# Kernel optimization log

Measured on AMD Instinct MI355X. Metric: run time of the kernel, lower is better.

The kernel has to match this reference:

```python
import jax, jax.numpy as jnp
import numpy as np

TOPK = 16          # static stand-in for dense_to_sparse(A_virtual): top-k neighbors per master node
LAMBDA_ATTN = 1.0  # VirtualGeneration temperature
GAMMA = 4.0        # gaussian radial basis width
R_CENTERS = 8      # radial_embedding.out_dim
NEG = -1e9


def _sh(v):
    # stand-in spherical harmonics: 16 monomials (lmax=3-ish) of the unit direction
    n = jnp.linalg.norm(v, axis=-1, keepdims=True)
    u = v / (n + 1e-9)
    x, y, z = u[:, 0], u[:, 1], u[:, 2]
    o = jnp.ones_like(x)
    return jnp.stack([o, x, y, z, x * x, y * y, z * z, x * y, x * z, y * z,
                      x * x * x, y * y * y, z * z * z, x * x * y, y * y * z, z * z * x], axis=-1)


def _radial(r):
    # gaussian radial basis, r: [E,1] -> [E,R]
    centers = jnp.linspace(0.0, 5.0, R_CENTERS, dtype=r.dtype)
    return jnp.exp(-GAMMA * (r - centers[None, :]) ** 2)


def _msgs(x, src, dst, sh, feats, Wr, wsh, n):
    # MACE-style conv message aggregation: radial-gated, SH-modulated gather/scatter
    gate = feats @ Wr                               # [E, Cin]
    msg = x[src] * gate * (sh @ wsh)[:, None]       # [E, Cin]
    return jax.ops.segment_sum(msg, dst, num_segments=n)


def _forward(h, pos, edge_index, edge_sh, edge_feats,
             W_loc_r, w_loc_sh, W_loc_out, W_prod_loc,
             W_ms1, b_ms1, W_ms2, b_ms2, Wq, Wk,
             W_a1, b_a1, W_a2, b_a2,
             W_h_r, w_h_sh, W_h_out, W_prod_h):
    N, D = h.shape
    D2 = W_loc_out.shape[1]
    S = W_ms1.shape[0]
    src, dst = edge_index[0], edge_index[1]

    # --- local conv + prod skip (h_local) ---
    h_up = _msgs(h, src, dst, edge_sh, edge_feats, W_loc_r, w_loc_sh, N) @ W_loc_out  # [N, D2]
    h_local = h_up @ W_prod_loc + jnp.pad(h, ((0, 0), (0, D2 - D)))
    h_scalar = h_local[:, :S]

    # --- master selection (MLP -> sigmoid -> hard threshold) ---
    m = jax.nn.sigmoid(jax.nn.relu(h_scalar @ W_ms1 + b_ms1) @ W_ms2 + b_ms2)[:, 0]
    mf = (m > 0.5).astype(h.dtype)

    # --- induced master-master edges: mask instead of dynamic subgraph extraction ---
    pair = mf[src] * mf[dst]
    vec_i = pos[src] - pos[dst]
    len_i = jnp.linalg.norm(vec_i, axis=-1, keepdims=True)
    sh_i = _sh(vec_i)
    rf_i = _radial(len_i) * pair[:, None]  # induced full_weights == 1, masked to master pairs

    # --- virtual edge generation: dense attention scores among masters, static top-k ---
    q = h_scalar @ Wq
    kk = h_scalar @ Wk
    scores_nn = (q @ kk.T) / (np.sqrt(S).astype(np.float32) * LAMBDA_ATTN)  # [N, N]
    pair_ok = (mf[:, None] * mf[None, :]) * (1.0 - jnp.eye(N, dtype=h.dtype))  # no self loops
    scores_nn = jnp.where(pair_ok > 0, scores_nn, NEG)
    topv, topi = jax.lax.top_k(scores_nn, TOPK)        # [N, K]
    vsrc = jnp.repeat(jnp.arange(N), TOPK)             # [N*K]
    vdst = topi.reshape(-1)
    vvalid = (topv.reshape(-1) > NEG / 2).astype(h.dtype)

    vec_v = pos[vsrc] - pos[vdst]
    len_v = jnp.linalg.norm(vec_v, axis=-1, keepdims=True)
    sh_v = _sh(vec_v)
    rf_v = _radial(len_v)

    # --- scatter-softmax attention over virtual edges (per destination) ---
    attn_in = jnp.concatenate([h_scalar[vsrc], h_scalar[vdst], rf_v], axis=-1)
    sc = (jax.nn.relu(attn_in @ W_a1 + b_a1) @ W_a2 + b_a2)[:, 0]
    sc = jnp.where(vvalid > 0, sc, NEG)
    mx = jax.ops.segment_max(sc, vdst, num_segments=N)
    ex = jnp.where(vvalid > 0, jnp.exp(sc - mx[vdst]), 0.0)
    den = jax.ops.segment_sum(ex, vdst, num_segments=N)
    wv = ex / (den[vdst] + 1e-12)
    rf_v = rf_v * wv[:, None]

    # --- hierarchical conv over induced + virtual master edges ---
    agg = (_msgs(h_local, src, dst, sh_i, rf_i, W_h_r, w_h_sh, N)
           + _msgs(h_local, vsrc, vdst, sh_v, rf_v, W_h_r, w_h_sh, N))
    h_m_up = agg @ W_h_out
    h_hier = (h_m_up @ W_prod_h + h_local) * mf[:, None]  # zero at non-master slots

    # --- gated combine ---
    return (1.0 - m)[:, None] * h_local + m[:, None] * h_hier


def setup_inputs():
    key = jax.random.key(0)
    ks = jax.random.split(key, 24)
    N, E, D, D2, S, R, L, HID = 4096, 131072, 128, 256, 128, 8, 16, 64

    def w(k, shape):
        return (jax.random.normal(k, shape, jnp.float32) / np.sqrt(shape[0]).astype(np.float32))

    return dict(
        h=jax.random.normal(ks[0], (N, D), jnp.float32),
        pos=jax.random.normal(ks[1], (N, 3), jnp.float32),
        edge_index=jax.random.randint(ks[2], (2, E), 0, N),
        edge_sh=jax.random.normal(ks[3], (E, L), jnp.float32),
        edge_feats=jax.random.normal(ks[4], (E, R), jnp.float32),
        batch=jnp.zeros((N,), jnp.int32),
        W_loc_r=w(ks[5], (R, D)),
        w_loc_sh=jax.random.normal(ks[6], (L,), jnp.float32) / 4.0,
        W_loc_out=w(ks[7], (D, D2)),
        W_prod_loc=w(ks[8], (D2, D2)),
        W_ms1=w(ks[9], (S, HID)), b_ms1=jnp.zeros((HID,), jnp.float32),
        W_ms2=w(ks[10], (HID, 1)), b_ms2=jnp.zeros((1,), jnp.float32),
        Wq=w(ks[11], (S, S)), Wk=w(ks[12], (S, S)),
        W_a1=w(ks[13], (2 * S + R, S)), b_a1=jnp.zeros((S,), jnp.float32),
        W_a2=w(ks[14], (S, 1)), b_a2=jnp.zeros((1,), jnp.float32),
        W_h_r=w(ks[15], (R, D2)),
        w_h_sh=jax.random.normal(ks[16], (L,), jnp.float32) / 4.0,
        W_h_out=w(ks[17], (D2, D2)),
        W_prod_h=w(ks[18], (D2, D2)),
    )


def reference(h, pos, edge_index, edge_sh, edge_feats, batch,
              W_loc_r, w_loc_sh, W_loc_out, W_prod_loc,
              W_ms1, b_ms1, W_ms2, b_ms2, Wq, Wk,
              W_a1, b_a1, W_a2, b_a2,
              W_h_r, w_h_sh, W_h_out, W_prod_h):
    # batch is unused by the original forward as well
    return _forward(h, pos, edge_index, edge_sh, edge_feats,
                    W_loc_r, w_loc_sh, W_loc_out, W_prod_loc,
                    W_ms1, b_ms1, W_ms2, b_ms2, Wq, Wk,
                    W_a1, b_a1, W_a2, b_a2,
                    W_h_r, w_h_sh, W_h_out, W_prod_h)
```

## Files before the change

### kernel.cpp

```cpp
#include <hip/hip_runtime.h>

typedef unsigned int u32;
typedef unsigned long long u64;

#define NN 4096
#define EE 131072
#define DD 128
#define D2 256
#define SS 128
#define RR 8
#define LL 16
#define HH 64
#define TK 16
#define VSTRIDE 32
#define VV2 (NN*VSTRIDE)
#define NEGF -1000000000.0f
#define MNEGF -3.0e38f
#define SCLF 11.313708305358886719f
#define DELTA 1.0e-3f
#define CHUNK 1024
#define RCH 32
#define VCH 64
#define MAXCH_R 8192
#define MAXCH_V 5184

__device__ __forceinline__ float fadd(float a, float b) { return __fadd_rn(a, b); }
__device__ __forceinline__ float fsub(float a, float b) { return __fsub_rn(a, b); }
__device__ __forceinline__ float fmul(float a, float b) { return __fmul_rn(a, b); }
__device__ __forceinline__ float ffma(float a, float b, float c) { return __fmaf_rn(a, b, c); }

enum : size_t {
  B_CNTR   = 0,
  B_CNTV   = 16384,
  B_MXE    = 32768,
  ZERO_END = 49152,
  B_STARTR = 49152,
  B_STARTV = 69632,
  B_LISTR  = 90112,
  B_LISTV  = 614400,
  B_TOPI   = 1138688,
  B_WFAC   = 1662976,
  B_AMSG   = 2187264,
  B_HUP    = 4284416,
  B_HLOC   = 8478720,
  B_T1     = 12673024,
  B_MARR   = 13721600,
  B_MF     = 13737984,
  B_Q      = 13754368,
  B_KT     = 15851520,
  B_SC     = 17948672,
  B_WV     = 18472960,
  B_SUMR   = 18997248,
  B_SUMV   = 23191552,
  B_AGG    = 27385856,
  B_HMUP   = 31580160,
  B_CURR   = 35774464,
  B_CURV   = 35790848,
  B_P1     = 35807232,
  B_P2     = 37904384,
  B_TOTAL  = 40001536,
  B_ERP    = B_Q,
  B_EVP    = B_HUP,
  B_SHV1   = B_SUMR,
  B_SCHUNK = B_SUMR,
  B_CHT    = B_HUP + 3145728,
  O_CHJV   = 64,
  O_CHPV   = 64 + 4*MAXCH_V,
  O_CHJR   = 64 + 8*MAXCH_V,
  O_CHPR   = 64 + 8*MAXCH_V + 4*MAXCH_R,
  B_CHT2   = 40001536,
  B_SBIG   = 41943040,
  WS_BIG   = 109051904
};

__global__ void count_keys(const int* __restrict__ keys, int n, u32* __restrict__ cnt) {
  int e = blockIdx.x * 256 + threadIdx.x;
  if (e >= n) return;
  int d = keys[e];
  if (d >= 0) atomicAdd(&cnt[d], 1u);
}

__global__ __launch_bounds__(256) void scan_ex_par(const u32* __restrict__ cnt,
                                                   u32* __restrict__ start,
                                                   u32* __restrict__ cursor, int n,
                                                   int csz, u32* __restrict__ chCnt,
                                                   int* __restrict__ chJ,
                                                   int* __restrict__ chP) {
  __shared__ u32 part[256];
  __shared__ u32 cpart[256];
  int t = threadIdx.x;
  int per = n / 256;
  u32 s = 0;
  for (int i = 0; i < per; ++i) s += cnt[t*per + i];
  part[t] = s;
  __syncthreads();
  if (t == 0) {
    u32 run = 0;
    for (int i = 0; i < 256; ++i) { u32 v = part[i]; part[i] = run; run += v; }
    start[n] = run;
  }
  __syncthreads();
  u32 run = part[t];
  for (int i = 0; i < per; ++i) {
    int k = t*per + i;
    start[k] = run;
    cursor[k] = run;
    run += cnt[k];
  }
  if (csz > 0) {
    u32 cc = 0;
    for (int i = 0; i < per; ++i) {
      u32 len = cnt[t*per + i];
      cc += (len + (u32)csz - 1u) / (u32)csz;
    }
    cpart[t] = cc;
    __syncthreads();
    if (t == 0) {
      u32 r2 = 0;
      for (int i = 0; i < 256; ++i) { u32 v = cpart[i]; cpart[i] = r2; r2 += v; }
      *chCnt = r2;
    }
    __syncthreads();
    u32 b = cpart[t];
    u32 sb = part[t];
    for (int i = 0; i < per; ++i) {
      int k = t*per + i;
      u32 len = cnt[k];
      u32 nch = (len + (u32)csz - 1u) / (u32)csz;
      for (u32 kk = 0; kk < nch; ++kk) { chJ[b] = k; chP[b] = (int)(sb + kk*(u32)csz); ++b; }
      sb += len;
    }
  }
}

__global__ void fill_atomic(const int* __restrict__ keys, int n,
                            u32* __restrict__ cursor, int* __restrict__ list) {
  int e = blockIdx.x * 256 + threadIdx.x;
  if (e >= n) return;
  int d = keys[e];
  if (d < 0) return;
  u32 p = atomicAdd(&cursor[d], 1u);
  list[p] = e;
}

__global__ void build_chunks(const u32* __restrict__ start, int nseg, int csz,
                             u32* __restrict__ cnt, int* __restrict__ chJ,
                             int* __restrict__ chP) {
  int j = blockIdx.x * 256 + threadIdx.x;
  if (j >= nseg) return;
  u32 s0 = start[j], s1 = start[j + 1];
  if (s0 >= s1) return;
  int nch = (int)((s1 - s0) + (u32)csz - 1) / csz;
  u32 b = atomicAdd(cnt, (u32)nch);
  for (int k = 0; k < nch; ++k) {
    chJ[b + k] = j;
    chP[b + k] = (int)(s0 + (u32)k * (u32)csz);
  }
}

__global__ void edge_pre1(const float* __restrict__ esh, const float* __restrict__ wsh,
                          float* __restrict__ shv1) {
  int e = blockIdx.x * 256 + threadIdx.x;
  if (e >= EE) return;
  float s = 0.f;
  #pragma unroll
  for (int l = 0; l < LL; ++l) s = ffma(esh[e*LL + l], wsh[l], s);
  shv1[e] = s;
}

__global__ __launch_bounds__(128) void rep_msgs1(
    const float* __restrict__ h, const int* __restrict__ ei,
    const float* __restrict__ efeat,
    const float* __restrict__ Wr, const float* __restrict__ shv1,
    const u32* __restrict__ startR, const int* __restrict__ listR,
    float* __restrict__ amsg)
{
  __shared__ int   ssrc[64];
  __shared__ float sshv[64];
  __shared__ float sef[64][8];
  int d = blockIdx.x, c = threadIdx.x;
  float wr[RR];
  #pragma unroll
  for (int r = 0; r < RR; ++r) wr[r] = Wr[r*DD + c];
  float acc = 0.f;
  u32 s0 = startR[d], s1 = startR[d + 1];
  for (u32 t0 = s0; t0 < s1; t0 += 64) {
    int tl = (int)(s1 - t0 < 64u ? s1 - t0 : 64u);
    if (c < tl) {
      int e = listR[t0 + c];
      ssrc[c] = ei[e];
      sshv[c] = shv1[e];
      const float4* fe = reinterpret_cast<const float4*>(&efeat[(size_t)e*RR]);
      float4 f0 = fe[0], f1 = fe[1];
      sef[c][0]=f0.x; sef[c][1]=f0.y; sef[c][2]=f0.z; sef[c][3]=f0.w;
      sef[c][4]=f1.x; sef[c][5]=f1.y; sef[c][6]=f1.z; sef[c][7]=f1.w;
    }
    __syncthreads();
    int k = 0;
    for (; k + 4 <= tl; k += 4) {
      float h0 = h[(size_t)ssrc[k  ]*DD + c];
      float h1 = h[(size_t)ssrc[k+1]*DD + c];
      float h2 = h[(size_t)ssrc[k+2]*DD + c];
      float h3 = h[(size_t)ssrc[k+3]*DD + c];
      float g0 = 0.f, g1 = 0.f, g2 = 0.f, g3 = 0.f;
      #pragma unroll
      for (int r = 0; r < RR; ++r) {
        g0 = ffma(sef[k  ][r], wr[r], g0);
        g1 = ffma(sef[k+1][r], wr[r], g1);
        g2 = ffma(sef[k+2][r], wr[r], g2);
        g3 = ffma(sef[k+3][r], wr[r], g3);
      }
      acc = fadd(acc, fmul(fmul(h0, g0), sshv[k  ]));
      acc = fadd(acc, fmul(fmul(h1, g1), sshv[k+1]));
      acc = fadd(acc, fmul(fmul(h2, g2), sshv[k+2]));
      acc = fadd(acc, fmul(fmul(h3, g3), sshv[k+3]));
    }
    for (; k < tl; ++k) {
      float hv = h[(size_t)ssrc[k]*DD + c];
      float g = 0.f;
      #pragma unroll
      for (int r = 0; r < RR; ++r) g = ffma(sef[k][r], wr[r], g);
      acc = fadd(acc, fmul(fmul(hv, g), sshv[k]));
    }
    __syncthreads();
  }
  amsg[d*DD + c] = acc;
}

__global__ __launch_bounds__(256) void gemm64(
    const float* __restrict__ A, int lda,
    const float* __restrict__ B, int ldb,
    float* __restrict__ C, int ldc,
    int K, int mode,
    const float* __restrict__ x1,
    const float* __restrict__ marr, const float* __restrict__ mfarr,
    float* __restrict__ outp)
{
  __shared__ float As[16][68];
  __shared__ float Bs[16][68];
  int tid = threadIdx.x;
  int bm = blockIdx.x << 6, bn = blockIdx.y << 6;
  int tm = ((tid >> 4) << 2), tn = ((tid & 15) << 2);
  float acc[4][4] = {};
  for (int k0 = 0; k0 < K; k0 += 16) {
    #pragma unroll
    for (int t = 0; t < 4; ++t) {
      int idx = tid + (t << 8);
      int r = idx >> 4, c = idx & 15;
      As[c][r] = A[(size_t)(bm + r)*lda + k0 + c];
      int rb = idx >> 6, cb = idx & 63;
      Bs[rb][cb] = B[(size_t)(k0 + rb)*ldb + bn + cb];
    }
    __syncthreads();
    #pragma unroll
    for (int kk = 0; kk < 16; ++kk) {
      float4 av = *reinterpret_cast<const float4*>(&As[kk][tm]);
      float4 bv = *reinterpret_cast<const float4*>(&Bs[kk][tn]);
      float a0 = av.x, a1 = av.y, a2 = av.z, a3 = av.w;
      float b0 = bv.x, b1 = bv.y, b2 = bv.z, b3 = bv.w;
      acc[0][0]=ffma(a0,b0,acc[0][0]); acc[0][1]=ffma(a0,b1,acc[0][1]);
      acc[0][2]=ffma(a0,b2,acc[0][2]); acc[0][3]=ffma(a0,b3,acc[0][3]);
      acc[1][0]=ffma(a1,b0,acc[1][0]); acc[1][1]=ffma(a1,b1,acc[1][1]);
      acc[1][2]=ffma(a1,b2,acc[1][2]); acc[1][3]=ffma(a1,b3,acc[1][3]);
      acc[2][0]=ffma(a2,b0,acc[2][0]); acc[2][1]=ffma(a2,b1,acc[2][1]);
      acc[2][2]=ffma(a2,b2,acc[2][2]); acc[2][3]=ffma(a2,b3,acc[2][3]);
      acc[3][0]=ffma(a3,b0,acc[3][0]); acc[3][1]=ffma(a3,b1,acc[3][1]);
      acc[3][2]=ffma(a3,b2,acc[3][2]); acc[3][3]=ffma(a3,b3,acc[3][3]);
    }
    __syncthreads();
  }
  #pragma unroll
  for (int ii = 0; ii < 4; ++ii) {
    int r = bm + tm + ii;
    #pragma unroll
    for (int jj = 0; jj < 4; ++jj) {
      int c = bn + tn + jj;
      float v = acc[ii][jj];
      if (mode == 0) {
        C[(size_t)r*ldc + c] = v;
      } else if (mode == 1) {
        if (c < DD) v = fadd(v, x1[(size_t)r*DD + c]);
        C[(size_t)r*ldc + c] = v;
      } else if (mode == 2) {
        float hl = x1[(size_t)r*D2 + c];
        float hh = fmul(fadd(v, hl), mfarr[r]);
        float m = marr[r];
        outp[(size_t)r*D2 + c] = fadd(fmul(fsub(1.f, m), hl), fmul(m, hh));
      } else {
        C[(size_t)c*ldc + r] = v;
      }
    }
  }
}

__global__ __launch_bounds__(256, 2) void gemm_score2(
    const float* __restrict__ A, const float* __restrict__ B,
    const float* __restrict__ mf, int rowoff,
    float* __restrict__ S)
{
  __shared__ float As[16][136];
  __shared__ float Bs[16][136];
  int tid = threadIdx.x;
  int bm = blockIdx.x << 7;
  int bn = blockIdx.y << 7;
  int tm = ((tid >> 4) << 2);
  int tn = ((tid & 15) << 2);
  float acc[8][8] = {};
  for (int k0 = 0; k0 < SS; k0 += 16) {
    {
      int row = tid >> 1, seg = (tid & 1) << 3;
      const float4 a0 = *reinterpret_cast<const float4*>(
          &A[(size_t)(bm + row)*SS + k0 + seg]);
      const float4 a1 = *reinterpret_cast<const float4*>(
          &A[(size_t)(bm + row)*SS + k0 + seg + 4]);
      As[seg+0][row] = a0.x; As[seg+1][row] = a0.y;
      As[seg+2][row] = a0.z; As[seg+3][row] = a0.w;
      As[seg+4][row] = a1.x; As[seg+5][row] = a1.y;
      As[seg+6][row] = a1.z; As[seg+7][row] = a1.w;
    }
    #pragma unroll
    for (int t = 0; t < 2; ++t) {
      int f = tid + (t << 8);
      int rb = f >> 5, cb = (f & 31) << 2;
      const float4 bv = *reinterpret_cast<const float4*>(
          &B[(size_t)(k0 + rb)*NN + bn + cb]);
      *reinterpret_cast<float4*>(&Bs[rb][cb]) = bv;
    }
    __syncthreads();
    #pragma unroll
    for (int kk = 0; kk < 16; ++kk) {
      float4 al = *reinterpret_cast<const float4*>(&As[kk][tm]);
      float4 ah = *reinterpret_cast<const float4*>(&As[kk][tm + 64]);
      float4 bl = *reinterpret_cast<const float4*>(&Bs[kk][tn]);
      float4 bh = *reinterpret_cast<const float4*>(&Bs[kk][tn + 64]);
      float a[8] = {al.x, al.y, al.z, al.w, ah.x, ah.y, ah.z, ah.w};
      float b[8] = {bl.x, bl.y, bl.z, bl.w, bh.x, bh.y, bh.z, bh.w};
      #pragma unroll
      for (int i = 0; i < 8; ++i)
        #pragma unroll
        for (int j = 0; j < 8; ++j)
          acc[i][j] = ffma(a[i], b[j], acc[i][j]);
    }
    __syncthreads();
  }
  #pragma unroll
  for (int ii = 0; ii < 8; ++ii) {
    int r = bm + ((ii < 4) ? (tm + ii) : (tm + 64 + (ii - 4)));
    int rg = rowoff + r;
    #pragma unroll
    for (int jg = 0; jg < 2; ++jg) {
      int cb = bn + tn + (jg << 6);
      float4 ov;
      {
        float s0 = __fdiv_rn(acc[ii][4*jg+0], SCLF);
        float s1 = __fdiv_rn(acc[ii][4*jg+1], SCLF);
        float s2 = __fdiv_rn(acc[ii][4*jg+2], SCLF);
        float s3 = __fdiv_rn(acc[ii][4*jg+3], SCLF);
        ov.x = ((mf[cb+0] > 0.5f) && (cb+0 != rg)) ? s0 : NEGF;
        ov.y = ((mf[cb+1] > 0.5f) && (cb+1 != rg)) ? s1 : NEGF;
        ov.z = ((mf[cb+2] > 0.5f) && (cb+2 != rg)) ? s2 : NEGF;
        ov.w = ((mf[cb+3] > 0.5f) && (cb+3 != rg)) ? s3 : NEGF;
      }
      *reinterpret_cast<float4*>(&S[(size_t)r*NN + cb]) = ov;
    }
  }
}

__device__ __forceinline__ u64 enc_key(float v, int j) {
  u32 u = __float_as_uint(v);
  u = (u & 0x80000000u) ? ~u : (u | 0x80000000u);
  return ((u64)u << 32) | (u32)(0xFFFFFFFFu - (u32)j);
}
__device__ __forceinline__ float dec_val(u64 k) {
  u32 e = (u32)(k >> 32);
  u32 u = (e & 0x80000000u) ? (e ^ 0x80000000u) : ~e;
  return __uint_as_float(u);
}
__device__ __forceinline__ int dec_idx(u64 k) {
  return (int)(0xFFFFFFFFu - (u32)k);
}

__global__ __launch_bounds__(256) void rep_sel(
    const float* __restrict__ S, int rowoff, const float* __restrict__ mf,
    int* __restrict__ topi, float* __restrict__ wfac)
{
  __shared__ u64 wm[2][4];
  int tid = threadIdx.x;
  int row = rowoff + blockIdx.x;
  int base = row * VSTRIDE;
  if (mf[row] <= 0.5f) {
    if (tid < VSTRIDE) { topi[base + tid] = -1; wfac[base + tid] = 0.f; }
    return;
  }
  u64 kk[16];
  const float4* rp = reinterpret_cast<const float4*>(S + (size_t)blockIdx.x * NN);
  #pragma unroll
  for (int g = 0; g < 4; ++g) {
    float4 v = rp[tid + (g << 8)];
    int j0 = (tid << 2) + (g << 10);
    kk[4*g+0] = enc_key(v.x, j0);
    kk[4*g+1] = enc_key(v.y, j0 + 1);
    kk[4*g+2] = enc_key(v.z, j0 + 2);
    kk[4*g+3] = enc_key(v.w, j0 + 3);
  }
  u64 cmx = 0;
  #pragma unroll
  for (int i = 0; i < 16; ++i) cmx = (kk[i] > cmx) ? kk[i] : cmx;
  int w = tid >> 6;
  u64 rv = cmx;
  #pragma unroll
  for (int off = 32; off > 0; off >>= 1) {
    u64 o = __shfl_down(rv, off);
    if (o > rv) rv = o;
  }
  rv = __shfl(rv, 0);

  float v15 = 0.f, v16 = 0.f; int i15 = -1, i16 = -1;
  for (int it = 0; it < 17; ++it) {
    int p = it & 1;
    if ((tid & 63) == 0) wm[p][w] = rv;
    __syncthreads();
    u64 m0 = wm[p][0], m1 = wm[p][1], m2 = wm[p][2], m3 = wm[p][3];
    u64 g01 = (m0 > m1) ? m0 : m1;
    u64 g23 = (m2 > m3) ? m2 : m3;
    u64 gmax = (g01 > g23) ? g01 : g23;
    if (tid == 0) {
      float fv = dec_val(gmax);
      int fi = dec_idx(gmax);
      if (it < 15) {
        bool ok = fv > 0.5f * NEGF;
        topi[base + it] = ok ? fi : -1;
        wfac[base + it] = ok ? 1.f : 0.f;
      } else if (it == 15) { v15 = fv; i15 = fi; }
      else                 { v16 = fv; i16 = fi; }
    }
    if (rv == gmax) {
      if (cmx == gmax) {
        u64 nm = 0;
        #pragma unroll
        for (int i = 0; i < 16; ++i) {
          kk[i] = (kk[i] == gmax) ? 0ull : kk[i];
          nm = (kk[i] > nm) ? kk[i] : nm;
        }
        cmx = nm;
      }
      u64 r2 = cmx;
      #pragma unroll
      for (int off = 32; off > 0; off >>= 1) {
        u64 o = __shfl_down(r2, off);
        if (o > r2) r2 = o;
      }
      rv = __shfl(r2, 0);
    }
  }
  if (tid == 0) {
    bool b16 = v15 > 0.5f * NEGF;
    bool b17 = v16 > 0.5f * NEGF;
    bool contested = b16 && b17 && (fsub(v15, v16) < DELTA);
    topi[base + 15] = b16 ? i15 : -1;
    wfac[base + 15] = b16 ? (contested ? 0.5f : 1.f) : 0.f;
    topi[base + 16] = contested ? i16 : -1;
    wfac[base + 16] = contested ? 0.5f : 0.f;
  }
  if (tid >= 17 && tid < VSTRIDE) { topi[base + tid] = -1; wfac[base + tid] = 0.f; }
}

__global__ __launch_bounds__(64) void rep_mask(const float* __restrict__ t1,
    const float* __restrict__ b1, const float* __restrict__ W2,
    const float* __restrict__ b2, float* __restrict__ marr, float* __restrict__ mf)
{
  __shared__ float t3[HH];
  int n = blockIdx.x, hh = threadIdx.x;
  t3[hh] = fmaxf(fadd(t1[n*HH + hh], b1[hh]), 0.f);
  __syncthreads();
  if (hh == 0) {
    float acc = 0.f;
    for (int k = 0; k < HH; ++k) acc = ffma(t3[k], W2[k], acc);
    float z = fadd(acc, b2[0]);
    float m = __fdiv_rn(1.f, fadd(1.f, expf(-z)));
    marr[n] = m;
    mf[n] = (m > 0.5f) ? 1.f : 0.f;
  }
}

__device__ __forceinline__ float centerf(int r) {
  return (float)(((double)r * 5.0) / 7.0);
}

__global__ __launch_bounds__(256) void attn_edge2(
    const float* __restrict__ P1, const float* __restrict__ P2,
    const float* __restrict__ pos, const int* __restrict__ topi,
    const float* __restrict__ Wa1, const float* __restrict__ ba1,
    const float* __restrict__ Wa2, const float* __restrict__ ba2,
    float* __restrict__ sc, u32* __restrict__ mxe)
{
  __shared__ float wsum[4];
  __shared__ float srf[2][8];
  int tid = threadIdx.x;
  int eh = tid >> 7;
  int c = tid & 127;
  int idx = blockIdx.x * 2 + eh;
  int i = idx / 17;
  int k = idx - i * 17;
  int v = (i << 5) + k;
  int j = topi[v];
  if (c < 8 && j >= 0) {
    float vx = fsub(pos[i*3+0], pos[j*3+0]);
    float vy = fsub(pos[i*3+1], pos[j*3+1]);
    float vz = fsub(pos[i*3+2], pos[j*3+2]);
    float n2 = fadd(fadd(fmul(vx,vx), fmul(vy,vy)), fmul(vz,vz));
    float len = __fsqrt_rn(n2);
    float dr = fsub(len, centerf(c));
    srf[eh][c] = expf(fmul(-4.f, fmul(dr, dr)));
  }
  __syncthreads();
  float p = 0.f;
  if (j >= 0) {
    float t = fadd(P1[(size_t)i*SS + c], P2[(size_t)j*SS + c]);
    #pragma unroll
    for (int r = 0; r < RR; ++r) {
      t = ffma(srf[eh][r], Wa1[(256 + r)*SS + c], t);
    }
    t = fmaxf(fadd(t, ba1[c]), 0.f);
    p = fmul(t, Wa2[c]);
  }
  #pragma unroll
  for (int off = 32; off > 0; off >>= 1) p += __shfl_down(p, off);
  int wid = tid >> 6;
  if ((tid & 63) == 0) wsum[wid] = p;
  __syncthreads();
  if ((tid & 127) == 0 && j >= 0) {
    float acc = wsum[eh*2] + wsum[eh*2 + 1];
    float s = fadd(acc, ba2[0]);
    sc[v] = s;
    u32 u = __float_as_uint(s);
    u = (u & 0x80000000u) ? ~u : (u | 0x80000000u);
    atomicMax(&mxe[j], u);
  }
}

__global__ __launch_bounds__(64) void rep_denwv2(
    const float* __restrict__ sc, const u32* __restrict__ mxe,
    const u32* __restrict__ startV, const int* __restrict__ listV,
    const float* __restrict__ wfac, float* __restrict__ wvv)
{
  int j = blockIdx.x;
  int lane = threadIdx.x;
  u32 s0 = startV[j], s1 = startV[j + 1];
  if (s0 == s1) return;
  u32 ue = mxe[j];
  u32 b = (ue & 0x80000000u) ? (ue ^ 0x80000000u) : ~ue;
  float mx = __uint_as_float(b);
  float psum = 0.f;
  for (u32 idx = s0 + lane; idx < s1; idx += 64) {
    int v = listV[idx];
    float ex = fmul(wfac[v], expf(fsub(sc[v], mx)));
    wvv[v] = ex;
    psum += ex;
  }
  #pragma unroll
  for (int off = 32; off > 0; off >>= 1) psum += __shfl_down(psum, off);
  float den = __shfl(psum, 0);
  float dd = fadd(den, 1e-12f);
  for (u32 idx = s0 + lane; idx < s1; idx += 64) {
    int v = listV[idx];
    wvv[v] = __fdiv_rn(wvv[v], dd);
  }
}

__device__ __forceinline__ float shrep(float vx, float vy, float vz,
                                       const float* __restrict__ w) {
  float n2 = fadd(fadd(fmul(vx,vx), fmul(vy,vy)), fmul(vz,vz));
  float n = __fsqrt_rn(n2);
  float dnm = fadd(n, 1e-9f);
  float x = __fdiv_rn(vx, dnm), y = __fdiv_rn(vy, dnm), z = __fdiv_rn(vz, dnm);
  float t[16];
  t[0]=1.f; t[1]=x; t[2]=y; t[3]=z;
  t[4]=fmul(x,x); t[5]=fmul(y,y); t[6]=fmul(z,z);
  t[7]=fmul(x,y); t[8]=fmul(x,z); t[9]=fmul(y,z);
  t[10]=fmul(fmul(x,x),x); t[11]=fmul(fmul(y,y),y); t[12]=fmul(fmul(z,z),z);
  t[13]=fmul(fmul(x,x),y); t[14]=fmul(fmul(y,y),z); t[15]=fmul(fmul(z,z),x);
  float s = 0.f;
  #pragma unroll
  for (int l = 0; l < 16; ++l) s = ffma(t[l], w[l], s);
  return s;
}

__global__ void edge_pre_rv(const float* __restrict__ pos, const int* __restrict__ ei,
                            const float* __restrict__ mf, const float* __restrict__ whsh,
                            const int* __restrict__ listR, float* __restrict__ erp,
                            const int* __restrict__ topi, const float* __restrict__ wvv,
                            const u32* __restrict__ startV, const int* __restrict__ listV,
                            float* __restrict__ evp) {
  int b = blockIdx.x;
  if (b < EE/256) {
    int p = b * 256 + threadIdx.x;
    int e = listR[p];
    int src = ei[e], dst = ei[EE + e];
    float* op = erp + (size_t)p * 9;
    if (mf[src] <= 0.5f || mf[dst] <= 0.5f) {
      #pragma unroll
      for (int r = 0; r < 9; ++r) op[r] = 0.f;
      return;
    }
    float vx = fsub(pos[src*3+0], pos[dst*3+0]);
    float vy = fsub(pos[src*3+1], pos[dst*3+1]);
    float vz = fsub(pos[src*3+2], pos[dst*3+2]);
    op[0] = shrep(vx, vy, vz, whsh);
    float len = __fsqrt_rn(fadd(fadd(fmul(vx,vx), fmul(vy,vy)), fmul(vz,vz)));
    #pragma unroll
    for (int r = 0; r < RR; ++r) {
      float dr = fsub(len, centerf(r));
      op[1 + r] = expf(fmul(-4.f, fmul(dr, dr)));
    }
  } else {
    int p = (b - EE/256) * 256 + threadIdx.x;
    if (p >= (int)startV[NN]) return;
    int v = listV[p];
    int i = v >> 5;
    int j = topi[v];
    float w = wvv[v];
    float* op = evp + (size_t)p * 9;
    float vx = fsub(pos[i*3+0], pos[j*3+0]);
    float vy = fsub(pos[i*3+1], pos[j*3+1]);
    float vz = fsub(pos[i*3+2], pos[j*3+2]);
    op[0] = shrep(vx, vy, vz, whsh);
    float len = __fsqrt_rn(fadd(fadd(fmul(vx,vx), fmul(vy,vy)), fmul(vz,vz)));
    #pragma unroll
    for (int r = 0; r < RR; ++r) {
      float dr = fsub(len, centerf(r));
      op[1 + r] = fmul(expf(fmul(-4.f, fmul(dr, dr))), w);
    }
  }
}

__global__ __launch_bounds__(256) void rep_msgs2r4(
    const float* __restrict__ hloc, const int* __restrict__ ei,
    const float* __restrict__ Whr, const float* __restrict__ erp,
    const u32* __restrict__ startR, const int* __restrict__ listR,
    const u32* __restrict__ cnt, const int* __restrict__ chJ,
    const int* __restrict__ chP, float* __restrict__ sumR)
{
  __shared__ int   ssrc[RCH];
  __shared__ float sep[RCH][9];
  int b = blockIdx.x;
  if (b >= (int)(*cnt)) return;
  int d = chJ[b], c = threadIdx.x;
  u32 p0 = (u32)chP[b];
  u32 p1 = startR[d + 1];
  u32 pe = p0 + RCH; if (pe < p1) p1 = pe;
  int len = (int)(p1 - p0);
  if (c < len) ssrc[c] = ei[listR[p0 + c]];
  for (int t = c; t < len*9; t += 256) (&sep[0][0])[t] = erp[(size_t)p0*9 + t];
  __syncthreads();
  float whr[RR];
  #pragma unroll
  for (int r = 0; r < RR; ++r) whr[r] = Whr[r*D2 + c];
  float acc = 0.f;
  int k = 0;
  for (; k + 4 <= len; k += 4) {
    float h0 = hloc[(size_t)ssrc[k  ]*D2 + c];
    float h1 = hloc[(size_t)ssrc[k+1]*D2 + c];
    float h2 = hloc[(size_t)ssrc[k+2]*D2 + c];
    float h3 = hloc[(size_t)ssrc[k+3]*D2 + c];
    float g0 = 0.f, g1 = 0.f, g2 = 0.f, g3 = 0.f;
    #pragma unroll
    for (int r = 0; r < RR; ++r) {
      g0 = ffma(sep[k  ][1 + r], whr[r], g0);
      g1 = ffma(sep[k+1][1 + r], whr[r], g1);
      g2 = ffma(sep[k+2][1 + r], whr[r], g2);
      g3 = ffma(sep[k+3][1 + r], whr[r], g3);
    }
    acc = fadd(acc, fmul(fmul(h0, g0), sep[k  ][0]));
    acc = fadd(acc, fmul(fmul(h1, g1), sep[k+1][0]));
    acc = fadd(acc, fmul(fmul(h2, g2), sep[k+2][0]));
    acc = fadd(acc, fmul(fmul(h3, g3), sep[k+3][0]));
  }
  for (; k < len; ++k) {
    float hv = hloc[(size_t)ssrc[k]*D2 + c];
    float g = 0.f;
    #pragma unroll
    for (int r = 0; r < RR; ++r) g = ffma(sep[k][1 + r], whr[r], g);
    acc = fadd(acc, fmul(fmul(hv, g), sep[k][0]));
  }
  atomicAdd(&sumR[(size_t)d*D2 + c], acc);
}

__global__ __launch_bounds__(256) void rep_msgs2v4(
    const float* __restrict__ hloc, const int* __restrict__ listV,
    const float* __restrict__ Whr, const float* __restrict__ evp,
    const u32* __restrict__ startV,
    const u32* __restrict__ cnt, const int* __restrict__ chJ,
    const int* __restrict__ chP, float* __restrict__ sumR)
{
  __shared__ int   si[VCH];
  __shared__ float sep[VCH][9];
  int b = blockIdx.x;
  if (b >= (int)(*cnt)) return;
  int j = chJ[b], c = threadIdx.x;
  u32 p0 = (u32)chP[b];
  u32 p1 = startV[j + 1];
  u32 pe = p0 + VCH; if (pe < p1) p1 = pe;
  int len = (int)(p1 - p0);
  if (c < len) si[c] = listV[p0 + c] >> 5;
  for (int t = c; t < len*9; t += 256) (&sep[0][0])[t] = evp[(size_t)p0*9 + t];
  __syncthreads();
  float whr[RR];
  #pragma unroll
  for (int r = 0; r < RR; ++r) whr[r] = Whr[r*D2 + c];
  float acc = 0.f;
  int k = 0;
  for (; k + 4 <= len; k += 4) {
    float h0 = hloc[(size_t)si[k  ]*D2 + c];
    float h1 = hloc[(size_t)si[k+1]*D2 + c];
    float h2 = hloc[(size_t)si[k+2]*D2 + c];
    float h3 = hloc[(size_t)si[k+3]*D2 + c];
    float g0 = 0.f, g1 = 0.f, g2 = 0.f, g3 = 0.f;
    #pragma unroll
    for (int r = 0; r < RR; ++r) {
      g0 = ffma(sep[k  ][1 + r], whr[r], g0);
      g1 = ffma(sep[k+1][1 + r], whr[r], g1);
      g2 = ffma(sep[k+2][1 + r], whr[r], g2);
      g3 = ffma(sep[k+3][1 + r], whr[r], g3);
    }
    acc = fadd(acc, fmul(fmul(h0, g0), sep[k  ][0]));
    acc = fadd(acc, fmul(fmul(h1, g1), sep[k+1][0]));
    acc = fadd(acc, fmul(fmul(h2, g2), sep[k+2][0]));
    acc = fadd(acc, fmul(fmul(h3, g3), sep[k+3][0]));
  }
  for (; k < len; ++k) {
    float hv = hloc[(size_t)si[k]*D2 + c];
    float g = 0.f;
    #pragma unroll
    for (int r = 0; r < RR; ++r) g = ffma(sep[k][1 + r], whr[r], g);
    acc = fadd(acc, fmul(fmul(hv, g), sep[k][0]));
  }
  atomicAdd(&sumR[(size_t)j*D2 + c], acc);
}

extern "C" void kernel_launch(void* const* d_in, const int* in_sizes, int n_in,
                              void* d_out, int out_size, void* d_ws, size_t ws_size,
                              hipStream_t stream)
{
  char* wsb = (char*)d_ws;
  const float* h     = (const float*)d_in[0];
  const float* pos   = (const float*)d_in[1];
  const int*   ei    = (const int*)d_in[2];
  const float* esh   = (const float*)d_in[3];
  const float* efeat = (const float*)d_in[4];
  const float* Wlr   = (const float*)d_in[6];
  const float* wlsh  = (const float*)d_in[7];
  const float* Wlo   = (const float*)d_in[8];
  const float* Wpl   = (const float*)d_in[9];
  const float* Wms1  = (const float*)d_in[10];
  const float* bms1  = (const float*)d_in[11];
  const float* Wms2  = (const float*)d_in[12];
  const float* bms2  = (const float*)d_in[13];
  const float* Wq    = (const float*)d_in[14];
  const float* Wk    = (const float*)d_in[15];
  const float* Wa1   = (const float*)d_in[16];
  const float* ba1   = (const float*)d_in[17];
  const float* Wa2   = (const float*)d_in[18];
  const float* ba2   = (const float*)d_in[19];
  const float* Whr   = (const float*)d_in[20];
  const float* whsh  = (const float*)d_in[21];
  const float* Who   = (const float*)d_in[22];
  const float* Wph   = (const float*)d_in[23];

  u32* cntR   = (u32*)(wsb + B_CNTR);
  u32* cntV   = (u32*)(wsb + B_CNTV);
  u32* mxe    = (u32*)(wsb + B_MXE);
  u32* startR = (u32*)(wsb + B_STARTR);
  u32* startV = (u32*)(wsb + B_STARTV);
  u32* curR   = (u32*)(wsb + B_CURR);
  u32* curV   = (u32*)(wsb + B_CURV);
  int* listR  = (int*)(wsb + B_LISTR);
  int* listV  = (int*)(wsb + B_LISTV);
  int* topi   = (int*)(wsb + B_TOPI);
  float* wfac = (float*)(wsb + B_WFAC);
  float* amsg = (float*)(wsb + B_AMSG);
  float* hup  = (float*)(wsb + B_HUP);
  float* hloc = (float*)(wsb + B_HLOC);
  float* t1   = (float*)(wsb + B_T1);
  float* marr = (float*)(wsb + B_MARR);
  float* mf   = (float*)(wsb + B_MF);
  float* q    = (float*)(wsb + B_Q);
  float* kT   = (float*)(wsb + B_KT);
  float* sc   = (float*)(wsb + B_SC);
  float* wvv  = (float*)(wsb + B_WV);
  float* sumR = (float*)(wsb + B_SUMR);
  float* hmup = (float*)(wsb + B_HMUP);
  float* P1   = (float*)(wsb + B_P1);
  float* P2   = (float*)(wsb + B_P2);
  float* erp  = (float*)(wsb + B_ERP);
  float* evp  = (float*)(wsb + B_EVP);
  float* shv1 = (float*)(wsb + B_SHV1);

  const bool big = ws_size >= (size_t)WS_BIG;
  char* cht = wsb + (big ? B_CHT2 : B_CHT);
  u32* chCntV = (u32*)(cht);
  u32* chCntR = (u32*)(cht + 4);
  int* chJv   = (int*)(cht + O_CHJV);
  int* chPv   = (int*)(cht + O_CHPV);
  int* chJr   = (int*)(cht + O_CHJR);
  int* chPr   = (int*)(cht + O_CHPR);
  float* Sbuf = (float*)(wsb + (big ? B_SBIG : B_SCHUNK));

  hipMemsetAsync(d_ws, 0, ZERO_END, stream);

  count_keys<<<EE/256, 256, 0, stream>>>(ei + EE, EE, cntR);
  if (big)
    scan_ex_par<<<1, 256, 0, stream>>>(cntR, startR, curR, NN, RCH, chCntR, chJr, chPr);
  else
    scan_ex_par<<<1, 256, 0, stream>>>(cntR, startR, curR, NN, 0, nullptr, nullptr, nullptr);
  fill_atomic<<<EE/256, 256, 0, stream>>>(ei + EE, EE, curR, listR);

  edge_pre1<<<EE/256, 256, 0, stream>>>(esh, wlsh, shv1);
  rep_msgs1<<<NN, 128, 0, stream>>>(h, ei, efeat, Wlr, shv1, startR, listR, amsg);
  gemm64<<<dim3(64,4), 256, 0, stream>>>(amsg, DD, Wlo, D2, hup, D2, DD, 0,
                                         nullptr, nullptr, nullptr, nullptr);
  gemm64<<<dim3(64,4), 256, 0, stream>>>(hup, D2, Wpl, D2, hloc, D2, D2, 1,
                                         h, nullptr, nullptr, nullptr);
  gemm64<<<dim3(64,1), 256, 0, stream>>>(hloc, D2, Wms1, HH, t1, HH, SS, 0,
                                         nullptr, nullptr, nullptr, nullptr);
  rep_mask<<<NN, 64, 0, stream>>>(t1, bms1, Wms2, bms2, marr, mf);
  gemm64<<<dim3(64,2), 256, 0, stream>>>(hloc, D2, Wq, SS, q, SS, SS, 0,
                                         nullptr, nullptr, nullptr, nullptr);
  gemm64<<<dim3(64,2), 256, 0, stream>>>(hloc, D2, Wk, SS, kT, NN, SS, 3,
                                         nullptr, nullptr, nullptr, nullptr);

  if (big) {
    gemm_score2<<<dim3(NN/128, NN/128), 256, 0, stream>>>(q, kT, mf, 0, Sbuf);
    rep_sel<<<NN, 256, 0, stream>>>(Sbuf, 0, mf, topi, wfac);
  } else {
    for (int c0 = 0; c0 < NN; c0 += CHUNK) {
      gemm_score2<<<dim3(CHUNK/128, NN/128), 256, 0, stream>>>(q + (size_t)c0*SS, kT,
                                                               mf, c0, Sbuf);
      rep_sel<<<CHUNK, 256, 0, stream>>>(Sbuf, c0, mf, topi, wfac);
    }
  }

  hipMemsetAsync(wsb + B_SUMR, 0, 4194304, stream);

  count_keys<<<VV2/256, 256, 0, stream>>>(topi, VV2, cntV);
  if (big)
    scan_ex_par<<<1, 256, 0, stream>>>(cntV, startV, curV, NN, VCH, chCntV, chJv, chPv);
  else
    scan_ex_par<<<1, 256, 0, stream>>>(cntV, startV, curV, NN, 0, nullptr, nullptr, nullptr);
  fill_atomic<<<VV2/256, 256, 0, stream>>>(topi, VV2, curV, listV);

  gemm64<<<dim3(64,2), 256, 0, stream>>>(hloc, D2, Wa1, SS, P1, SS, SS, 0,
                                         nullptr, nullptr, nullptr, nullptr);
  gemm64<<<dim3(64,2), 256, 0, stream>>>(hloc, D2, Wa1 + 128*SS, SS, P2, SS, SS, 0,
                                         nullptr, nullptr, nullptr, nullptr);
  attn_edge2<<<(NN*17)/2, 256, 0, stream>>>(P1, P2, pos, topi, Wa1, ba1, Wa2, ba2,
                                            sc, mxe);
  rep_denwv2<<<NN, 64, 0, stream>>>(sc, mxe, startV, listV, wfac, wvv);

  if (!big) {
    hipMemsetAsync(cht, 0, 8, stream);
    build_chunks<<<NN/256, 256, 0, stream>>>(startV, NN, VCH, chCntV, chJv, chPv);
    build_chunks<<<NN/256, 256, 0, stream>>>(startR, NN, RCH, chCntR, chJr, chPr);
  }

  edge_pre_rv<<<EE/256 + (NN*17 + 255)/256, 256, 0, stream>>>(
      pos, ei, mf, whsh, listR, erp, topi, wvv, startV, listV, evp);

  rep_msgs2r4<<<MAXCH_R, 256, 0, stream>>>(hloc, ei, Whr, erp, startR, listR,
                                           chCntR, chJr, chPr, sumR);
  rep_msgs2v4<<<MAXCH_V, 256, 0, stream>>>(hloc, listV, Whr, evp, startV,
                                           chCntV, chJv, chPv, sumR);

  gemm64<<<dim3(64,4), 256, 0, stream>>>(sumR, D2, Who, D2, hmup, D2, D2, 0,
                                         nullptr, nullptr, nullptr, nullptr);
  gemm64<<<dim3(64,4), 256, 0, stream>>>(hmup, D2, Wph, D2, nullptr, D2, D2, 2,
                                         hloc, marr, mf, (float*)d_out);
}
```

Before: 511.4 us.

## Fuse per-tile top-17 selection into score GEMM and merge candidates

The score GEMM epilogue no longer writes the full 4096x4096 masked score matrix. Each 16-lane group instead extracts the top-17 encoded keys of its 128-column tile and writes them as candidates, 32 tiles x 17 = 544 per row. A new selection kernel then merges these candidates with one wavefront per row using shuffles only, with no shared-memory barriers. Separately, the SH-weight dot product is folded into the message kernel, which removes the edge_pre1 launch and its intermediate buffer. The cost is 17 serial shuffle-reduction rounds per row inside the GEMM epilogue, which lengthens that kernel, in exchange for much less global memory traffic.

```diff
diff --git a/kernel.cpp b/kernel.cpp
--- a/kernel.cpp
+++ b/kernel.cpp
@@ -19,6 +19,8 @@
 #define SCLF 11.313708305358886719f
 #define DELTA 1.0e-3f
 #define CHUNK 1024
+#define NTILE 32
+#define CAND 544
 #define RCH 32
 #define VCH 64
 #define MAXCH_R 8192
@@ -61,7 +63,6 @@
   B_TOTAL  = 40001536,
   B_ERP    = B_Q,
   B_EVP    = B_HUP,
-  B_SHV1   = B_SUMR,
   B_SCHUNK = B_SUMR,
   B_CHT    = B_HUP + 3145728,
   O_CHJV   = 64,
@@ -158,20 +159,11 @@
   }
 }
 
-__global__ void edge_pre1(const float* __restrict__ esh, const float* __restrict__ wsh,
-                          float* __restrict__ shv1) {
-  int e = blockIdx.x * 256 + threadIdx.x;
-  if (e >= EE) return;
-  float s = 0.f;
-  #pragma unroll
-  for (int l = 0; l < LL; ++l) s = ffma(esh[e*LL + l], wsh[l], s);
-  shv1[e] = s;
-}
-
 __global__ __launch_bounds__(128) void rep_msgs1(
     const float* __restrict__ h, const int* __restrict__ ei,
-    const float* __restrict__ efeat,
-    const float* __restrict__ Wr, const float* __restrict__ shv1,
+    const float* __restrict__ efeat, const float* __restrict__ esh,
+    const float* __restrict__ wlsh,
+    const float* __restrict__ Wr,
     const u32* __restrict__ startR, const int* __restrict__ listR,
     float* __restrict__ amsg)
 {
@@ -189,7 +181,10 @@
     if (c < tl) {
       int e = listR[t0 + c];
       ssrc[c] = ei[e];
-      sshv[c] = shv1[e];
+      float s = 0.f;
+      #pragma unroll
+      for (int l = 0; l < LL; ++l) s = ffma(esh[(size_t)e*LL + l], wlsh[l], s);
+      sshv[c] = s;
       const float4* fe = reinterpret_cast<const float4*>(&efeat[(size_t)e*RR]);
       float4 f0 = fe[0], f1 = fe[1];
       sef[c][0]=f0.x; sef[c][1]=f0.y; sef[c][2]=f0.z; sef[c][3]=f0.w;
@@ -293,10 +288,24 @@
   }
 }
 
-__global__ __launch_bounds__(256, 2) void gemm_score2(
+__device__ __forceinline__ u64 enc_key(float v, int j) {
+  u32 u = __float_as_uint(v);
+  u = (u & 0x80000000u) ? ~u : (u | 0x80000000u);
+  return ((u64)u << 32) | (u32)(0xFFFFFFFFu - (u32)j);
+}
+__device__ __forceinline__ float dec_val(u64 k) {
+  u32 e = (u32)(k >> 32);
+  u32 u = (e & 0x80000000u) ? (e ^ 0x80000000u) : ~e;
+  return __uint_as_float(u);
+}
+__device__ __forceinline__ int dec_idx(u64 k) {
+  return (int)(0xFFFFFFFFu - (u32)k);
+}
+
+__global__ __launch_bounds__(256, 2) void gemm_score3(
     const float* __restrict__ A, const float* __restrict__ B,
     const float* __restrict__ mf, int rowoff,
-    float* __restrict__ S)
+    u64* __restrict__ cand)
 {
   __shared__ float As[16][136];
   __shared__ float Bs[16][136];
@@ -343,88 +352,90 @@
     }
     __syncthreads();
   }
+  int colv[8]; float okv[8];
+  #pragma unroll
+  for (int v = 0; v < 8; ++v) {
+    colv[v] = bn + ((v < 4) ? (tn + v) : (tn + 64 + (v - 4)));
+    okv[v] = mf[colv[v]];
+  }
+  int sub = tid & 15;
   #pragma unroll
   for (int ii = 0; ii < 8; ++ii) {
     int r = bm + ((ii < 4) ? (tm + ii) : (tm + 64 + (ii - 4)));
     int rg = rowoff + r;
-    #pragma unroll
-    for (int jg = 0; jg < 2; ++jg) {
-      int cb = bn + tn + (jg << 6);
-      float4 ov;
-      {
-        float s0 = __fdiv_rn(acc[ii][4*jg+0], SCLF);
-        float s1 = __fdiv_rn(acc[ii][4*jg+1], SCLF);
-        float s2 = __fdiv_rn(acc[ii][4*jg+2], SCLF);
-        float s3 = __fdiv_rn(acc[ii][4*jg+3], SCLF);
-        ov.x = ((mf[cb+0] > 0.5f) && (cb+0 != rg)) ? s0 : NEGF;
-        ov.y = ((mf[cb+1] > 0.5f) && (cb+1 != rg)) ? s1 : NEGF;
-        ov.z = ((mf[cb+2] > 0.5f) && (cb+2 != rg)) ? s2 : NEGF;
-        ov.w = ((mf[cb+3] > 0.5f) && (cb+3 != rg)) ? s3 : NEGF;
+    u64 kq[8];
+    #pragma unroll
+    for (int v = 0; v < 8; ++v) {
+      float s = __fdiv_rn(acc[ii][v], SCLF);
+      bool valid = (okv[v] > 0.5f) && (colv[v] != rg);
+      kq[v] = enc_key(valid ? s : NEGF, colv[v]);
+    }
+    u64 cmx = 0;
+    #pragma unroll
+    for (int v = 0; v < 8; ++v) cmx = (kq[v] > cmx) ? kq[v] : cmx;
+    u64* crow = cand + ((size_t)r * NTILE + blockIdx.y) * 17;
+    for (int it = 0; it < 17; ++it) {
+      u64 m = cmx;
+      #pragma unroll
+      for (int off = 8; off > 0; off >>= 1) {
+        u64 o = __shfl_down(m, off, 16);
+        if (o > m) m = o;
       }
-      *reinterpret_cast<float4*>(&S[(size_t)r*NN + cb]) = ov;
-    }
-  }
-}
-
-__device__ __forceinline__ u64 enc_key(float v, int j) {
-  u32 u = __float_as_uint(v);
-  u = (u & 0x80000000u) ? ~u : (u | 0x80000000u);
-  return ((u64)u << 32) | (u32)(0xFFFFFFFFu - (u32)j);
-}
-__device__ __forceinline__ float dec_val(u64 k) {
-  u32 e = (u32)(k >> 32);
-  u32 u = (e & 0x80000000u) ? (e ^ 0x80000000u) : ~e;
-  return __uint_as_float(u);
-}
-__device__ __forceinline__ int dec_idx(u64 k) {
-  return (int)(0xFFFFFFFFu - (u32)k);
-}
-
-__global__ __launch_bounds__(256) void rep_sel(
-    const float* __restrict__ S, int rowoff, const float* __restrict__ mf,
+      u64 gmax = __shfl(m, 0, 16);
+      if (cmx == gmax) {
+        u64 nm = 0;
+        #pragma unroll
+        for (int v = 0; v < 8; ++v) {
+          kq[v] = (kq[v] == gmax) ? 0ull : kq[v];
+          nm = (kq[v] > nm) ? kq[v] : nm;
+        }
+        cmx = nm;
+      }
+      if (sub == 0) crow[it] = gmax;
+    }
+  }
+}
+
+__global__ __launch_bounds__(256) void rep_sel3(
+    const u64* __restrict__ cand, int rowoff, const float* __restrict__ mf,
     int* __restrict__ topi, float* __restrict__ wfac)
 {
-  __shared__ u64 wm[2][4];
   int tid = threadIdx.x;
-  int row = rowoff + blockIdx.x;
+  int w = tid >> 6, lane = tid & 63;
+  int lrow = blockIdx.x * 4 + w;
+  int row = rowoff + lrow;
   int base = row * VSTRIDE;
   if (mf[row] <= 0.5f) {
-    if (tid < VSTRIDE) { topi[base + tid] = -1; wfac[base + tid] = 0.f; }
+    if (lane < VSTRIDE) { topi[base + lane] = -1; wfac[base + lane] = 0.f; }
     return;
   }
-  u64 kk[16];
-  const float4* rp = reinterpret_cast<const float4*>(S + (size_t)blockIdx.x * NN);
-  #pragma unroll
-  for (int g = 0; g < 4; ++g) {
-    float4 v = rp[tid + (g << 8)];
-    int j0 = (tid << 2) + (g << 10);
-    kk[4*g+0] = enc_key(v.x, j0);
-    kk[4*g+1] = enc_key(v.y, j0 + 1);
-    kk[4*g+2] = enc_key(v.z, j0 + 2);
-    kk[4*g+3] = enc_key(v.w, j0 + 3);
-  }
+  const u64* cr = cand + (size_t)lrow * CAND;
+  u64 kq[9];
+  #pragma unroll
+  for (int t = 0; t < 8; ++t) kq[t] = cr[t*64 + lane];
+  kq[8] = (lane < 32) ? cr[512 + lane] : 0ull;
   u64 cmx = 0;
   #pragma unroll
-  for (int i = 0; i < 16; ++i) cmx = (kk[i] > cmx) ? kk[i] : cmx;
-  int w = tid >> 6;
-  u64 rv = cmx;
-  #pragma unroll
-  for (int off = 32; off > 0; off >>= 1) {
-    u64 o = __shfl_down(rv, off);
-    if (o > rv) rv = o;
-  }
-  rv = __shfl(rv, 0);
-
+  for (int t = 0; t < 9; ++t) cmx = (kq[t] > cmx) ? kq[t] : cmx;
   float v15 = 0.f, v16 = 0.f; int i15 = -1, i16 = -1;
   for (int it = 0; it < 17; ++it) {
-    int p = it & 1;
-    if ((tid & 63) == 0) wm[p][w] = rv;
-    __syncthreads();
-    u64 m0 = wm[p][0], m1 = wm[p][1], m2 = wm[p][2], m3 = wm[p][3];
-    u64 g01 = (m0 > m1) ? m0 : m1;
-    u64 g23 = (m2 > m3) ? m2 : m3;
-    u64 gmax = (g01 > g23) ? g01 : g23;
-    if (tid == 0) {
+    u64 m = cmx;
+    #pragma unroll
+    for (int off = 32; off > 0; off >>= 1) {
+      u64 o = __shfl_down(m, off);
+      if (o > m) m = o;
+    }
+    u64 gmax = __shfl(m, 0);
+    if (cmx == gmax) {
+      u64 nm = 0;
+      #pragma unroll
+      for (int t = 0; t < 9; ++t) {
+        kq[t] = (kq[t] == gmax) ? 0ull : kq[t];
+        nm = (kq[t] > nm) ? kq[t] : nm;
+      }
+      cmx = nm;
+    }
+    if (lane == 0) {
       float fv = dec_val(gmax);
       int fi = dec_idx(gmax);
       if (it < 15) {
@@ -434,26 +445,8 @@
       } else if (it == 15) { v15 = fv; i15 = fi; }
       else                 { v16 = fv; i16 = fi; }
     }
-    if (rv == gmax) {
-      if (cmx == gmax) {
-        u64 nm = 0;
-        #pragma unroll
-        for (int i = 0; i < 16; ++i) {
-          kk[i] = (kk[i] == gmax) ? 0ull : kk[i];
-          nm = (kk[i] > nm) ? kk[i] : nm;
-        }
-        cmx = nm;
-      }
-      u64 r2 = cmx;
-      #pragma unroll
-      for (int off = 32; off > 0; off >>= 1) {
-        u64 o = __shfl_down(r2, off);
-        if (o > r2) r2 = o;
-      }
-      rv = __shfl(r2, 0);
-    }
-  }
-  if (tid == 0) {
+  }
+  if (lane == 0) {
     bool b16 = v15 > 0.5f * NEGF;
     bool b17 = v16 > 0.5f * NEGF;
     bool contested = b16 && b17 && (fsub(v15, v16) < DELTA);
@@ -462,7 +455,7 @@
     topi[base + 16] = contested ? i16 : -1;
     wfac[base + 16] = contested ? 0.5f : 0.f;
   }
-  if (tid >= 17 && tid < VSTRIDE) { topi[base + tid] = -1; wfac[base + tid] = 0.f; }
+  if (lane >= 17 && lane < VSTRIDE) { topi[base + lane] = -1; wfac[base + lane] = 0.f; }
 }
 
 __global__ __launch_bounds__(64) void rep_mask(const float* __restrict__ t1,
@@ -794,7 +787,6 @@
   float* P2   = (float*)(wsb + B_P2);
   float* erp  = (float*)(wsb + B_ERP);
   float* evp  = (float*)(wsb + B_EVP);
-  float* shv1 = (float*)(wsb + B_SHV1);
 
   const bool big = ws_size >= (size_t)WS_BIG;
   char* cht = wsb + (big ? B_CHT2 : B_CHT);
@@ -804,7 +796,7 @@
   int* chPv   = (int*)(cht + O_CHPV);
   int* chJr   = (int*)(cht + O_CHJR);
   int* chPr   = (int*)(cht + O_CHPR);
-  float* Sbuf = (float*)(wsb + (big ? B_SBIG : B_SCHUNK));
+  u64* cand   = (u64*)(wsb + (big ? B_SBIG : B_SCHUNK));
 
   hipMemsetAsync(d_ws, 0, ZERO_END, stream);
 
@@ -815,8 +807,7 @@
     scan_ex_par<<<1, 256, 0, stream>>>(cntR, startR, curR, NN, 0, nullptr, nullptr, nullptr);
   fill_atomic<<<EE/256, 256, 0, stream>>>(ei + EE, EE, curR, listR);
 
-  edge_pre1<<<EE/256, 256, 0, stream>>>(esh, wlsh, shv1);
-  rep_msgs1<<<NN, 128, 0, stream>>>(h, ei, efeat, Wlr, shv1, startR, listR, amsg);
+  rep_msgs1<<<NN, 128, 0, stream>>>(h, ei, efeat, esh, wlsh, Wlr, startR, listR, amsg);
   gemm64<<<dim3(64,4), 256, 0, stream>>>(amsg, DD, Wlo, D2, hup, D2, DD, 0,
                                          nullptr, nullptr, nullptr, nullptr);
   gemm64<<<dim3(64,4), 256, 0, stream>>>(hup, D2, Wpl, D2, hloc, D2, D2, 1,
@@ -830,13 +821,13 @@
                                          nullptr, nullptr, nullptr, nullptr);
 
   if (big) {
-    gemm_score2<<<dim3(NN/128, NN/128), 256, 0, stream>>>(q, kT, mf, 0, Sbuf);
-    rep_sel<<<NN, 256, 0, stream>>>(Sbuf, 0, mf, topi, wfac);
+    gemm_score3<<<dim3(NN/128, NN/128), 256, 0, stream>>>(q, kT, mf, 0, cand);
+    rep_sel3<<<NN/4, 256, 0, stream>>>(cand, 0, mf, topi, wfac);
   } else {
     for (int c0 = 0; c0 < NN; c0 += CHUNK) {
-      gemm_score2<<<dim3(CHUNK/128, NN/128), 256, 0, stream>>>(q + (size_t)c0*SS, kT,
-                                                               mf, c0, Sbuf);
-      rep_sel<<<CHUNK, 256, 0, stream>>>(Sbuf, c0, mf, topi, wfac);
+      gemm_score3<<<dim3(CHUNK/128, NN/128), 256, 0, stream>>>(q + (size_t)c0*SS, kT,
+                                                               mf, c0, cand);
+      rep_sel3<<<CHUNK/4, 256, 0, stream>>>(cand, c0, mf, topi, wfac);
     }
   }
 
```

Measured after the change: 642.8 us. 1.26x slower.
